# Kernel tuning notes

Measured on AMD Instinct MI355X. Metric: run time of the kernel, lower is better.

The kernel has to match this reference:

```python
import jax, jax.numpy as jnp
import numpy as np

N_NODES = 50000
N_EDGES = 800000
D_IN = 128
HIDDEN = [128, 128]
D_OUT = 64


def setup_inputs() -> dict:
    key = jax.random.key(0)
    ks = jax.random.split(key, 12)
    x = jax.random.normal(ks[0], (N_NODES, D_IN), dtype=jnp.float32)
    edge_index = jax.random.randint(ks[1], (2, N_EDGES), 0, N_NODES, dtype=jnp.int64)
    # SAGEConv params: lin_l acts on aggregated neighbors (has bias), lin_r on root
    def lin(k, fan_in, fan_out):
        s = 1.0 / np.sqrt(fan_in)
        return jax.random.uniform(k, (fan_in, fan_out), jnp.float32, -s, s)
    dims = [D_IN] + HIDDEN
    inp = {"x": x, "edge_index": edge_index}
    for i in range(len(HIDDEN)):
        inp[f"Wl{i}"] = lin(ks[2 + 3 * i], dims[i], dims[i + 1])
        inp[f"Wr{i}"] = lin(ks[3 + 3 * i], dims[i], dims[i + 1])
        inp[f"b{i}"] = jnp.zeros((dims[i + 1],), jnp.float32)
    inp["Wfc"] = lin(ks[10], HIDDEN[-1], D_OUT)
    inp["bfc"] = jnp.zeros((D_OUT,), jnp.float32)
    return inp


def _sage_conv(x, src, dst, n, Wl, Wr, b, deg_inv):
    # mean-aggregate source features into destination nodes
    agg = jax.ops.segment_sum(x[src], dst, num_segments=n) * deg_inv[:, None]
    return agg @ Wl + x @ Wr + b


def reference(x, edge_index, Wl0, Wr0, b0, Wl1, Wr1, b1, Wfc, bfc):
    src, dst = edge_index[0], edge_index[1]
    n = x.shape[0]
    deg = jax.ops.segment_sum(jnp.ones((src.shape[0],), x.dtype), dst, num_segments=n)
    deg_inv = 1.0 / jnp.maximum(deg, 1.0)
    h = jax.nn.relu(_sage_conv(x, src, dst, n, Wl0, Wr0, b0, deg_inv))
    # dropout p=0 / eval mode -> identity
    h = jax.nn.relu(_sage_conv(h, src, dst, n, Wl1, Wr1, b1, deg_inv))
    return h @ Wfc + bfc
```

## Files before the change

kernel.cpp:

```cpp
#include <hip/hip_runtime.h>
#include <hip/hip_bf16.h>

#define NN 50000
#define NE 800000
#define D 128
#define DOUT 64
#define PAD 64
#define BSH 8
#define NBUCK 196
#define CAP 4608
#define CHUNK 4096
#define N8 (NN * D / 8)

typedef __attribute__((ext_vector_type(8))) short short8;
typedef __attribute__((ext_vector_type(4))) float float4v;


__device__ inline unsigned short f2bf(float f) {
    union { float f; unsigned int i; } c; c.f = f;
    unsigned int u = c.i;
    return (unsigned short)((u + 0x7fffu + ((u >> 16) & 1u)) >> 16);
}
__device__ inline float bflo(unsigned int u) {
    union { unsigned int i; float f; } c; c.i = u << 16; return c.f;
}
__device__ inline float bfhi(unsigned int u) {
    union { unsigned int i; float f; } c; c.i = u & 0xffff0000u; return c.f;
}


struct PrepArgs {
    const float* W[5];
    unsigned short* P[5];
    int* gcur;
    const float* x;
    unsigned short* xb;
    unsigned short* zrow;
};

__global__ void prep(PrepArgs args) {
    int b = blockIdx.x;
    if (b < 36) {
        int idx = b * 256 + threadIdx.x;
        const float* W;
        unsigned short* P;
        int COLS, local;
        if (idx < 4 * 2048) {
            int wsel = idx >> 11;
            W = args.W[wsel]; P = args.P[wsel]; COLS = 128; local = idx & 2047;
        } else {
            W = args.W[4]; P = args.P[4]; COLS = 64; local = idx - 4 * 2048;
        }
        int CT = COLS >> 4;
        int lane = local & 63;
        int fi = local >> 6;
        int ct = fi % CT;
        int kstep = fi / CT;
        int krow = kstep * 32 + (lane >> 4) * 8;
        int col = ct * 16 + (lane & 15);
        unsigned short v[8];
#pragma unroll
        for (int j = 0; j < 8; ++j) v[j] = f2bf(W[(size_t)(krow + j) * COLS + col]);
        unsigned int w0 = v[0] | ((unsigned int)v[1] << 16);
        unsigned int w1 = v[2] | ((unsigned int)v[3] << 16);
        unsigned int w2 = v[4] | ((unsigned int)v[5] << 16);
        unsigned int w3 = v[6] | ((unsigned int)v[7] << 16);
        *(uint4*)(P + (size_t)local * 8) = make_uint4(w0, w1, w2, w3);
    } else if (b == 36) {
        if (threadIdx.x < NBUCK) args.gcur[threadIdx.x] = 0;
        if (threadIdx.x >= 224 && threadIdx.x < 240)
            *(uint4*)(args.zrow + (size_t)(threadIdx.x - 224) * 8) = make_uint4(0, 0, 0, 0);
    } else {
        int stride = (gridDim.x - 37) * 256;
        for (int i = (b - 37) * 256 + threadIdx.x; i < N8; i += stride) {
            const float4* p = (const float4*)args.x + (size_t)i * 2;
            float4 a = p[0], bb = p[1];
            unsigned int w0 = f2bf(a.x) | ((unsigned int)f2bf(a.y) << 16);
            unsigned int w1 = f2bf(a.z) | ((unsigned int)f2bf(a.w) << 16);
            unsigned int w2 = f2bf(bb.x) | ((unsigned int)f2bf(bb.y) << 16);
            unsigned int w3 = f2bf(bb.z) | ((unsigned int)f2bf(bb.w) << 16);
            *(uint4*)(args.xb + (size_t)i * 8) = make_uint4(w0, w1, w2, w3);
        }
    }
}


__global__ void bin_edges(const int* __restrict__ src, const int* __restrict__ dst,
                          int* __restrict__ gcur, unsigned int* __restrict__ binned, int e) {
    __shared__ int cnt[NBUCK];
    __shared__ int sh[256];
    __shared__ int baseg[NBUCK];
    __shared__ int lcur[NBUCK];
    __shared__ unsigned int buf[CHUNK];
    int tid = threadIdx.x;
    int base = blockIdx.x * CHUNK;
    for (int b = tid; b < NBUCK; b += 256) cnt[b] = 0;
    __syncthreads();
    unsigned int rec[16];
#pragma unroll
    for (int i = 0; i < 16; ++i) {
        int ei = base + i * 256 + tid;
        rec[i] = 0xffffffffu;
        if (ei < e) {
            unsigned int d = (unsigned int)dst[ei];
            unsigned int s = (unsigned int)src[ei];
            rec[i] = (d << 16) | s;
            atomicAdd(&cnt[d >> BSH], 1);
        }
    }
    __syncthreads();
    int v = (tid < NBUCK) ? cnt[tid] : 0;
    sh[tid] = v;
    __syncthreads();
    for (int off = 1; off < 256; off <<= 1) {
        int t = (tid >= off) ? sh[tid - off] : 0;
        __syncthreads();
        sh[tid] += t;
        __syncthreads();
    }
    if (tid < NBUCK) {
        baseg[tid] = atomicAdd(&gcur[tid], cnt[tid]);
        lcur[tid] = sh[tid] - cnt[tid];
    }
    __syncthreads();
    int total = sh[255];
#pragma unroll
    for (int i = 0; i < 16; ++i) {
        if (rec[i] != 0xffffffffu) {
            int b = rec[i] >> 24;
            int pos = atomicAdd(&lcur[b], 1);
            buf[pos] = rec[i];
        }
    }
    __syncthreads();
    for (int j = tid; j < total; j += 256) {
        unsigned int r = buf[j];
        int b = r >> 24;
        int gidx = baseg[b] + (j - (sh[b] - cnt[b]));
        if (gidx < CAP) binned[(size_t)b * CAP + gidx] = r;
    }
}


__global__ void scatter_bucket(const unsigned int* __restrict__ binned, const int* __restrict__ gcur,
                               unsigned short* __restrict__ eidx_pad, int* __restrict__ cursor) {
    __shared__ int cur[256];
    int b = blockIdx.x;
    int tid = threadIdx.x;
    if (tid < 256) cur[tid] = 0;
    __syncthreads();
    int count = gcur[b];
    if (count > CAP) count = CAP;
    const unsigned int* seg = binned + (size_t)b * CAP;
    for (int j = tid; j < count; j += 512) {
        unsigned int r = seg[j];
        int dl = (r >> 16) & 255;
        int slot = atomicAdd(&cur[dl], 1);
        if (slot < PAD)
            eidx_pad[((size_t)((b << BSH) + dl)) * PAD + slot] = (unsigned short)(r & 0xffffu);
    }
    __syncthreads();
    if (tid < 256) {
        int node = (b << BSH) + tid;
        if (node < NN) cursor[node] = (cur[tid] < PAD) ? cur[tid] : PAD;
    }
}


template <bool FUSEFC>
__global__ __launch_bounds__(256, 4)
void fused_layer(const unsigned short* __restrict__ feat,
                 const int* __restrict__ cursor, const unsigned short* __restrict__ eidx_pad,
                 const unsigned short* __restrict__ zrow,
                 const unsigned short* __restrict__ Pl, const unsigned short* __restrict__ Pr,
                 const float* __restrict__ bias,
                 const unsigned short* __restrict__ Pfc, const float* __restrict__ bfc,
                 unsigned short* __restrict__ outb, float* __restrict__ outf, int n) {
    __shared__ __align__(16) unsigned short As[64][136];

    int tid = threadIdx.x;
    int row0 = blockIdx.x * 64;

    {
        int g = tid >> 4;
        int l = tid & 15;
        int nbase = row0 + g * 4;
        int4 dv = *(const int4*)(cursor + nbase);
        const unsigned short* rbase = eidx_pad + (size_t)nbase * PAD;
        uint4 ia = *(const uint4*)(rbase);
        uint4 ib = *(const uint4*)(rbase + 8);
#pragma unroll
        for (int nn = 0; nn < 4; ++nn) {
            int r = g * 4 + nn;
            int node = nbase + nn;
            uint4 ca = ia, cb = ib;
            if (nn < 3) {
                ia = *(const uint4*)(rbase + (nn + 1) * PAD);
                ib = *(const uint4*)(rbase + (nn + 1) * PAD + 8);
            }
            int deg = 0;
            if (node < n) deg = ((const int*)&dv)[nn];
            float di = 1.0f / (float)(deg > 1 ? deg : 1);
            float acc[8] = {0.f, 0.f, 0.f, 0.f, 0.f, 0.f, 0.f, 0.f};
            {
                int id[16];
                id[0] = ca.x & 0xffff;  id[1] = ca.x >> 16;
                id[2] = ca.y & 0xffff;  id[3] = ca.y >> 16;
                id[4] = ca.z & 0xffff;  id[5] = ca.z >> 16;
                id[6] = ca.w & 0xffff;  id[7] = ca.w >> 16;
                id[8] = cb.x & 0xffff;  id[9] = cb.x >> 16;
                id[10] = cb.y & 0xffff; id[11] = cb.y >> 16;
                id[12] = cb.z & 0xffff; id[13] = cb.z >> 16;
                id[14] = cb.w & 0xffff; id[15] = cb.w >> 16;
                uint4 v[16];
#pragma unroll
                for (int k = 0; k < 16; ++k) {
                    const unsigned short* sp = (k < deg) ? (feat + (size_t)id[k] * D) : zrow;
                    v[k] = *(const uint4*)(sp + l * 8);
                }
#pragma unroll
                for (int k = 0; k < 16; ++k) {
                    acc[0] += bflo(v[k].x); acc[1] += bfhi(v[k].x);
                    acc[2] += bflo(v[k].y); acc[3] += bfhi(v[k].y);
                    acc[4] += bflo(v[k].z); acc[5] += bfhi(v[k].z);
                    acc[6] += bflo(v[k].w); acc[7] += bfhi(v[k].w);
                }
                const unsigned short* rowp = rbase + nn * PAD;
                int p = 16;
                while (p < deg) {
                    uint4 iv = *(const uint4*)(rowp + p);
                    int jd[8];
                    jd[0] = iv.x & 0xffff; jd[1] = iv.x >> 16;
                    jd[2] = iv.y & 0xffff; jd[3] = iv.y >> 16;
                    jd[4] = iv.z & 0xffff; jd[5] = iv.z >> 16;
                    jd[6] = iv.w & 0xffff; jd[7] = iv.w >> 16;
                    uint4 w[8];
#pragma unroll
                    for (int k = 0; k < 8; ++k) {
                        const unsigned short* sp = (p + k < deg) ? (feat + (size_t)jd[k] * D) : zrow;
                        w[k] = *(const uint4*)(sp + l * 8);
                    }
#pragma unroll
                    for (int k = 0; k < 8; ++k) {
                        acc[0] += bflo(w[k].x); acc[1] += bfhi(w[k].x);
                        acc[2] += bflo(w[k].y); acc[3] += bfhi(w[k].y);
                        acc[4] += bflo(w[k].z); acc[5] += bfhi(w[k].z);
                        acc[6] += bflo(w[k].w); acc[7] += bfhi(w[k].w);
                    }
                    p += 8;
                }
            }
            unsigned int w0 = f2bf(acc[0] * di) | ((unsigned int)f2bf(acc[1] * di) << 16);
            unsigned int w1 = f2bf(acc[2] * di) | ((unsigned int)f2bf(acc[3] * di) << 16);
            unsigned int w2 = f2bf(acc[4] * di) | ((unsigned int)f2bf(acc[5] * di) << 16);
            unsigned int w3 = f2bf(acc[6] * di) | ((unsigned int)f2bf(acc[7] * di) << 16);
            *(uint4*)&As[r][l * 8] = make_uint4(w0, w1, w2, w3);
        }
    }

    int wave = tid >> 6;
    int lane = tid & 63;
    int m16 = lane & 15;
    int quad = lane >> 4;
    int rt0 = (wave & 1) * 32;
    int ctb = (wave >> 1) * 4;

    float4v acc[2][4];
#pragma unroll
    for (int t = 0; t < 2; ++t)
#pragma unroll
        for (int c = 0; c < 4; ++c) acc[t][c] = (float4v){0.f, 0.f, 0.f, 0.f};

#pragma unroll
    for (int ks = 0; ks < 4; ++ks) {
        short8 xf[2];
#pragma unroll
        for (int t = 0; t < 2; ++t) {
            int row = row0 + rt0 + t * 16 + m16;
            short8 z = {0, 0, 0, 0, 0, 0, 0, 0};
            xf[t] = (row < n) ? *(const short8*)(feat + (size_t)row * D + ks * 32 + quad * 8) : z;
        }
#pragma unroll
        for (int c = 0; c < 4; ++c) {
            short8 bf = *(const short8*)(Pr + ((size_t)((ks * 8 + ctb + c) * 64 + lane)) * 8);
#pragma unroll
            for (int t = 0; t < 2; ++t)
                acc[t][c] = __builtin_amdgcn_mfma_f32_16x16x32_bf16(xf[t], bf, acc[t][c], 0, 0, 0);
        }
    }

    __syncthreads();

#pragma unroll
    for (int ks = 0; ks < 4; ++ks) {
        short8 af[2];
#pragma unroll
        for (int t = 0; t < 2; ++t)
            af[t] = *(const short8*)&As[rt0 + t * 16 + m16][ks * 32 + quad * 8];
#pragma unroll
        for (int c = 0; c < 4; ++c) {
            short8 bf = *(const short8*)(Pl + ((size_t)((ks * 8 + ctb + c) * 64 + lane)) * 8);
#pragma unroll
            for (int t = 0; t < 2; ++t)
                acc[t][c] = __builtin_amdgcn_mfma_f32_16x16x32_bf16(af[t], bf, acc[t][c], 0, 0, 0);
        }
    }

    if (!FUSEFC) {
#pragma unroll
        for (int t = 0; t < 2; ++t) {
#pragma unroll
            for (int c = 0; c < 4; ++c) {
                int col = (ctb + c) * 16 + m16;
                float bv = bias[col];
#pragma unroll
                for (int i = 0; i < 4; ++i) {
                    int row = row0 + rt0 + t * 16 + quad * 4 + i;
                    if (row < n)
                        outb[(size_t)row * D + col] = f2bf(fmaxf(acc[t][c][i] + bv, 0.f));
                }
            }
        }
    } else {
        __syncthreads();
#pragma unroll
        for (int t = 0; t < 2; ++t) {
#pragma unroll
            for (int c = 0; c < 4; ++c) {
                int col = (ctb + c) * 16 + m16;
                float bv = bias[col];
#pragma unroll
                for (int i = 0; i < 4; ++i) {
                    int row = rt0 + t * 16 + quad * 4 + i;
                    As[row][col] = f2bf(fmaxf(acc[t][c][i] + bv, 0.f));
                }
            }
        }
        __syncthreads();

        int ctbF = (wave >> 1) * 2;
        float4v acc2[2][2];
#pragma unroll
        for (int t = 0; t < 2; ++t)
#pragma unroll
            for (int c = 0; c < 2; ++c) acc2[t][c] = (float4v){0.f, 0.f, 0.f, 0.f};
#pragma unroll
        for (int ks = 0; ks < 4; ++ks) {
            short8 hf[2];
#pragma unroll
            for (int t = 0; t < 2; ++t)
                hf[t] = *(const short8*)&As[rt0 + t * 16 + m16][ks * 32 + quad * 8];
#pragma unroll
            for (int c = 0; c < 2; ++c) {
                short8 bf = *(const short8*)(Pfc + ((size_t)((ks * 4 + ctbF + c) * 64 + lane)) * 8);
#pragma unroll
                for (int t = 0; t < 2; ++t)
                    acc2[t][c] = __builtin_amdgcn_mfma_f32_16x16x32_bf16(hf[t], bf, acc2[t][c], 0, 0, 0);
            }
        }
#pragma unroll
        for (int t = 0; t < 2; ++t) {
#pragma unroll
            for (int c = 0; c < 2; ++c) {
                int col = (ctbF + c) * 16 + m16;
                float bv = bfc[col];
#pragma unroll
                for (int i = 0; i < 4; ++i) {
                    int row = row0 + rt0 + t * 16 + quad * 4 + i;
                    if (row < n)
                        outf[(size_t)row * DOUT + col] = acc2[t][c][i] + bv;
                }
            }
        }
    }
}


extern "C" void kernel_launch(void* const* d_in, const int* in_sizes, int n_in,
                              void* d_out, int out_size, void* d_ws, size_t ws_size,
                              hipStream_t stream) {
    const float* x   = (const float*)d_in[0];
    const int*   ei  = (const int*)d_in[1];
    const float* Wl0 = (const float*)d_in[2];
    const float* Wr0 = (const float*)d_in[3];
    const float* b0  = (const float*)d_in[4];
    const float* Wl1 = (const float*)d_in[5];
    const float* Wr1 = (const float*)d_in[6];
    const float* b1  = (const float*)d_in[7];
    const float* Wfc = (const float*)d_in[8];
    const float* bfc = (const float*)d_in[9];
    float* out = (float*)d_out;

    const int* src = ei;
    const int* dst = ei + NE;

    char* p = (char*)d_ws;
    auto carve = [&](size_t bytes) {
        char* q = p;
        p += (bytes + 255) & ~(size_t)255;
        return q;
    };
    int*            cursor   = (int*)carve(NN * sizeof(int));
    int*            gcur     = (int*)carve(NBUCK * sizeof(int));
    unsigned short* zrow     = (unsigned short*)carve(256);
    unsigned int*   binned   = (unsigned int*)carve((size_t)NBUCK * CAP * 4);
    unsigned short* eidx_pad = (unsigned short*)carve((size_t)NN * PAD * 2);
    unsigned short* xb   = (unsigned short*)carve((size_t)NN * D * 2);
    unsigned short* h0b  = (unsigned short*)carve((size_t)NN * D * 2);
    unsigned short* Wl0p = (unsigned short*)carve(D * D * 2);
    unsigned short* Wr0p = (unsigned short*)carve(D * D * 2);
    unsigned short* Wl1p = (unsigned short*)carve(D * D * 2);
    unsigned short* Wr1p = (unsigned short*)carve(D * D * 2);
    unsigned short* Wfcp = (unsigned short*)carve(D * DOUT * 2);

    PrepArgs pa;
    pa.W[0] = Wl0; pa.W[1] = Wr0; pa.W[2] = Wl1; pa.W[3] = Wr1; pa.W[4] = Wfc;
    pa.P[0] = Wl0p; pa.P[1] = Wr0p; pa.P[2] = Wl1p; pa.P[3] = Wr1p; pa.P[4] = Wfcp;
    pa.gcur = gcur;
    pa.x = x; pa.xb = xb;
    pa.zrow = zrow;
    prep<<<256, 256, 0, stream>>>(pa);

    const int BINB = (NE + CHUNK - 1) / CHUNK;
    bin_edges<<<BINB, 256, 0, stream>>>(src, dst, gcur, binned, NE);
    scatter_bucket<<<NBUCK, 512, 0, stream>>>(binned, gcur, eidx_pad, cursor);

    const int GB = (NN + 63) / 64;

    fused_layer<false><<<GB, 256, 0, stream>>>(xb, cursor, eidx_pad, zrow, Wl0p, Wr0p, b0,
                                               nullptr, nullptr, h0b, nullptr, NN);
    fused_layer<true><<<GB, 256, 0, stream>>>(h0b, cursor, eidx_pad, zrow, Wl1p, Wr1p, b1,
                                              Wfcp, bfc, nullptr, out, NN);
}
```

Baseline: 187.0 us.

## Merge prep and edge binning into one kernel using per-block bucket segments

Edge binning now writes each block's bucket records into a fixed-size private segment (SEGC slots per block per bucket) with per-block counts, instead of reserving space through global atomics on a gcur counter. That removes the need to zero gcur beforehand, so the binning blocks and the weight/x bf16 conversion blocks are folded into a single launch, dropping one kernel boundary. scatter_bucket then walks every block segment for its bucket, which adds some strided, partly empty reads. Edges beyond SEGC in any block/bucket pair are silently dropped, which is a correctness risk if a bucket gets skewed.

```diff
diff --git a/kernel.cpp b/kernel.cpp
--- a/kernel.cpp
+++ b/kernel.cpp
@@ -8,8 +8,9 @@
 #define PAD 64
 #define BSH 8
 #define NBUCK 196
-#define CAP 4608
 #define CHUNK 4096
+#define NBINB 196
+#define SEGC 56
 #define N8 (NN * D / 8)
 
 typedef __attribute__((ext_vector_type(8))) short short8;
@@ -29,139 +30,143 @@
 }
 
 
-struct PrepArgs {
+struct Stage1Args {
+    const int* src;
+    const int* dst;
+    unsigned int* binned;
+    int* cnts;
     const float* W[5];
     unsigned short* P[5];
-    int* gcur;
     const float* x;
     unsigned short* xb;
     unsigned short* zrow;
 };
 
-__global__ void prep(PrepArgs args) {
-    int b = blockIdx.x;
-    if (b < 36) {
-        int idx = b * 256 + threadIdx.x;
-        const float* W;
-        unsigned short* P;
-        int COLS, local;
-        if (idx < 4 * 2048) {
-            int wsel = idx >> 11;
-            W = args.W[wsel]; P = args.P[wsel]; COLS = 128; local = idx & 2047;
+__global__ void stage1(Stage1Args args) {
+    int blk = blockIdx.x;
+    int tid = threadIdx.x;
+    if (blk < NBINB) {
+        __shared__ int cnt[NBUCK];
+        __shared__ int sh[256];
+        __shared__ int lcur[NBUCK];
+        __shared__ unsigned int buf[CHUNK];
+        int base = blk * CHUNK;
+        for (int b = tid; b < NBUCK; b += 256) cnt[b] = 0;
+        __syncthreads();
+        unsigned int rec[16];
+#pragma unroll
+        for (int i = 0; i < 16; ++i) {
+            int ei = base + i * 256 + tid;
+            rec[i] = 0xffffffffu;
+            if (ei < NE) {
+                unsigned int d = (unsigned int)args.dst[ei];
+                unsigned int s = (unsigned int)args.src[ei];
+                rec[i] = (d << 16) | s;
+                atomicAdd(&cnt[d >> BSH], 1);
+            }
+        }
+        __syncthreads();
+        int v = (tid < NBUCK) ? cnt[tid] : 0;
+        sh[tid] = v;
+        __syncthreads();
+        for (int off = 1; off < 256; off <<= 1) {
+            int t = (tid >= off) ? sh[tid - off] : 0;
+            __syncthreads();
+            sh[tid] += t;
+            __syncthreads();
+        }
+        if (tid < NBUCK) {
+            lcur[tid] = sh[tid] - cnt[tid];
+            args.cnts[blk * NBUCK + tid] = (cnt[tid] < SEGC) ? cnt[tid] : SEGC;
+        }
+        __syncthreads();
+        int total = sh[255];
+#pragma unroll
+        for (int i = 0; i < 16; ++i) {
+            if (rec[i] != 0xffffffffu) {
+                int b = rec[i] >> 24;
+                int pos = atomicAdd(&lcur[b], 1);
+                buf[pos] = rec[i];
+            }
+        }
+        __syncthreads();
+        for (int j = tid; j < total; j += 256) {
+            unsigned int r = buf[j];
+            int q = r >> 24;
+            int k = j - (sh[q] - cnt[q]);
+            if (k < SEGC)
+                args.binned[((size_t)q * NBINB + blk) * SEGC + k] = r;
+        }
+    } else {
+        int b = blk - NBINB;
+        if (b < 36) {
+            int idx = b * 256 + tid;
+            const float* W;
+            unsigned short* P;
+            int COLS, local;
+            if (idx < 4 * 2048) {
+                int wsel = idx >> 11;
+                W = args.W[wsel]; P = args.P[wsel]; COLS = 128; local = idx & 2047;
+            } else {
+                W = args.W[4]; P = args.P[4]; COLS = 64; local = idx - 4 * 2048;
+            }
+            int CT = COLS >> 4;
+            int lane = local & 63;
+            int fi = local >> 6;
+            int ct = fi % CT;
+            int kstep = fi / CT;
+            int krow = kstep * 32 + (lane >> 4) * 8;
+            int col = ct * 16 + (lane & 15);
+            unsigned short v[8];
+#pragma unroll
+            for (int j = 0; j < 8; ++j) v[j] = f2bf(W[(size_t)(krow + j) * COLS + col]);
+            unsigned int w0 = v[0] | ((unsigned int)v[1] << 16);
+            unsigned int w1 = v[2] | ((unsigned int)v[3] << 16);
+            unsigned int w2 = v[4] | ((unsigned int)v[5] << 16);
+            unsigned int w3 = v[6] | ((unsigned int)v[7] << 16);
+            *(uint4*)(P + (size_t)local * 8) = make_uint4(w0, w1, w2, w3);
+            if (b == 0 && tid < 16)
+                *(uint4*)(args.zrow + (size_t)tid * 8) = make_uint4(0, 0, 0, 0);
         } else {
-            W = args.W[4]; P = args.P[4]; COLS = 64; local = idx - 4 * 2048;
-        }
-        int CT = COLS >> 4;
-        int lane = local & 63;
-        int fi = local >> 6;
-        int ct = fi % CT;
-        int kstep = fi / CT;
-        int krow = kstep * 32 + (lane >> 4) * 8;
-        int col = ct * 16 + (lane & 15);
-        unsigned short v[8];
-#pragma unroll
-        for (int j = 0; j < 8; ++j) v[j] = f2bf(W[(size_t)(krow + j) * COLS + col]);
-        unsigned int w0 = v[0] | ((unsigned int)v[1] << 16);
-        unsigned int w1 = v[2] | ((unsigned int)v[3] << 16);
-        unsigned int w2 = v[4] | ((unsigned int)v[5] << 16);
-        unsigned int w3 = v[6] | ((unsigned int)v[7] << 16);
-        *(uint4*)(P + (size_t)local * 8) = make_uint4(w0, w1, w2, w3);
-    } else if (b == 36) {
-        if (threadIdx.x < NBUCK) args.gcur[threadIdx.x] = 0;
-        if (threadIdx.x >= 224 && threadIdx.x < 240)
-            *(uint4*)(args.zrow + (size_t)(threadIdx.x - 224) * 8) = make_uint4(0, 0, 0, 0);
-    } else {
-        int stride = (gridDim.x - 37) * 256;
-        for (int i = (b - 37) * 256 + threadIdx.x; i < N8; i += stride) {
-            const float4* p = (const float4*)args.x + (size_t)i * 2;
-            float4 a = p[0], bb = p[1];
-            unsigned int w0 = f2bf(a.x) | ((unsigned int)f2bf(a.y) << 16);
-            unsigned int w1 = f2bf(a.z) | ((unsigned int)f2bf(a.w) << 16);
-            unsigned int w2 = f2bf(bb.x) | ((unsigned int)f2bf(bb.y) << 16);
-            unsigned int w3 = f2bf(bb.z) | ((unsigned int)f2bf(bb.w) << 16);
-            *(uint4*)(args.xb + (size_t)i * 8) = make_uint4(w0, w1, w2, w3);
-        }
-    }
-}
-
-
-__global__ void bin_edges(const int* __restrict__ src, const int* __restrict__ dst,
-                          int* __restrict__ gcur, unsigned int* __restrict__ binned, int e) {
-    __shared__ int cnt[NBUCK];
-    __shared__ int sh[256];
-    __shared__ int baseg[NBUCK];
-    __shared__ int lcur[NBUCK];
-    __shared__ unsigned int buf[CHUNK];
-    int tid = threadIdx.x;
-    int base = blockIdx.x * CHUNK;
-    for (int b = tid; b < NBUCK; b += 256) cnt[b] = 0;
-    __syncthreads();
-    unsigned int rec[16];
-#pragma unroll
-    for (int i = 0; i < 16; ++i) {
-        int ei = base + i * 256 + tid;
-        rec[i] = 0xffffffffu;
-        if (ei < e) {
-            unsigned int d = (unsigned int)dst[ei];
-            unsigned int s = (unsigned int)src[ei];
-            rec[i] = (d << 16) | s;
-            atomicAdd(&cnt[d >> BSH], 1);
-        }
-    }
-    __syncthreads();
-    int v = (tid < NBUCK) ? cnt[tid] : 0;
-    sh[tid] = v;
-    __syncthreads();
-    for (int off = 1; off < 256; off <<= 1) {
-        int t = (tid >= off) ? sh[tid - off] : 0;
-        __syncthreads();
-        sh[tid] += t;
-        __syncthreads();
-    }
-    if (tid < NBUCK) {
-        baseg[tid] = atomicAdd(&gcur[tid], cnt[tid]);
-        lcur[tid] = sh[tid] - cnt[tid];
-    }
-    __syncthreads();
-    int total = sh[255];
-#pragma unroll
-    for (int i = 0; i < 16; ++i) {
-        if (rec[i] != 0xffffffffu) {
-            int b = rec[i] >> 24;
-            int pos = atomicAdd(&lcur[b], 1);
-            buf[pos] = rec[i];
-        }
-    }
-    __syncthreads();
-    for (int j = tid; j < total; j += 256) {
-        unsigned int r = buf[j];
-        int b = r >> 24;
-        int gidx = baseg[b] + (j - (sh[b] - cnt[b]));
-        if (gidx < CAP) binned[(size_t)b * CAP + gidx] = r;
-    }
-}
-
-
-__global__ void scatter_bucket(const unsigned int* __restrict__ binned, const int* __restrict__ gcur,
+            int stride = (gridDim.x - NBINB - 36) * 256;
+            for (int i = (b - 36) * 256 + tid; i < N8; i += stride) {
+                const float4* p = (const float4*)args.x + (size_t)i * 2;
+                float4 a = p[0], bb = p[1];
+                unsigned int w0 = f2bf(a.x) | ((unsigned int)f2bf(a.y) << 16);
+                unsigned int w1 = f2bf(a.z) | ((unsigned int)f2bf(a.w) << 16);
+                unsigned int w2 = f2bf(bb.x) | ((unsigned int)f2bf(bb.y) << 16);
+                unsigned int w3 = f2bf(bb.z) | ((unsigned int)f2bf(bb.w) << 16);
+                *(uint4*)(args.xb + (size_t)i * 8) = make_uint4(w0, w1, w2, w3);
+            }
+        }
+    }
+}
+
+
+__global__ void scatter_bucket(const unsigned int* __restrict__ binned, const int* __restrict__ cnts,
                                unsigned short* __restrict__ eidx_pad, int* __restrict__ cursor) {
     __shared__ int cur[256];
-    int b = blockIdx.x;
+    __shared__ int segc[NBINB];
+    int q = blockIdx.x;
     int tid = threadIdx.x;
     if (tid < 256) cur[tid] = 0;
+    for (int s = tid; s < NBINB; s += 512) segc[s] = cnts[(size_t)s * NBUCK + q];
     __syncthreads();
-    int count = gcur[b];
-    if (count > CAP) count = CAP;
-    const unsigned int* seg = binned + (size_t)b * CAP;
-    for (int j = tid; j < count; j += 512) {
-        unsigned int r = seg[j];
-        int dl = (r >> 16) & 255;
-        int slot = atomicAdd(&cur[dl], 1);
-        if (slot < PAD)
-            eidx_pad[((size_t)((b << BSH) + dl)) * PAD + slot] = (unsigned short)(r & 0xffffu);
+    const unsigned int* bq = binned + (size_t)q * NBINB * SEGC;
+    for (int idx = tid; idx < NBINB * SEGC; idx += 512) {
+        int seg = idx / SEGC;
+        int k = idx - seg * SEGC;
+        if (k < segc[seg]) {
+            unsigned int r = bq[(size_t)seg * SEGC + k];
+            int dl = (r >> 16) & 255;
+            int slot = atomicAdd(&cur[dl], 1);
+            if (slot < PAD)
+                eidx_pad[((size_t)((q << BSH) + dl)) * PAD + slot] = (unsigned short)(r & 0xffffu);
+        }
     }
     __syncthreads();
     if (tid < 256) {
-        int node = (b << BSH) + tid;
+        int node = (q << BSH) + tid;
         if (node < NN) cursor[node] = (cur[tid] < PAD) ? cur[tid] : PAD;
     }
 }
@@ -401,9 +406,9 @@
         return q;
     };
     int*            cursor   = (int*)carve(NN * sizeof(int));
-    int*            gcur     = (int*)carve(NBUCK * sizeof(int));
+    int*            cnts     = (int*)carve((size_t)NBINB * NBUCK * sizeof(int));
     unsigned short* zrow     = (unsigned short*)carve(256);
-    unsigned int*   binned   = (unsigned int*)carve((size_t)NBUCK * CAP * 4);
+    unsigned int*   binned   = (unsigned int*)carve((size_t)NBUCK * NBINB * SEGC * 4);
     unsigned short* eidx_pad = (unsigned short*)carve((size_t)NN * PAD * 2);
     unsigned short* xb   = (unsigned short*)carve((size_t)NN * D * 2);
     unsigned short* h0b  = (unsigned short*)carve((size_t)NN * D * 2);
@@ -413,17 +418,15 @@
     unsigned short* Wr1p = (unsigned short*)carve(D * D * 2);
     unsigned short* Wfcp = (unsigned short*)carve(D * DOUT * 2);
 
-    PrepArgs pa;
-    pa.W[0] = Wl0; pa.W[1] = Wr0; pa.W[2] = Wl1; pa.W[3] = Wr1; pa.W[4] = Wfc;
-    pa.P[0] = Wl0p; pa.P[1] = Wr0p; pa.P[2] = Wl1p; pa.P[3] = Wr1p; pa.P[4] = Wfcp;
-    pa.gcur = gcur;
-    pa.x = x; pa.xb = xb;
-    pa.zrow = zrow;
-    prep<<<256, 256, 0, stream>>>(pa);
-
-    const int BINB = (NE + CHUNK - 1) / CHUNK;
-    bin_edges<<<BINB, 256, 0, stream>>>(src, dst, gcur, binned, NE);
-    scatter_bucket<<<NBUCK, 512, 0, stream>>>(binned, gcur, eidx_pad, cursor);
+    Stage1Args sa;
+    sa.src = src; sa.dst = dst;
+    sa.binned = binned; sa.cnts = cnts;
+    sa.W[0] = Wl0; sa.W[1] = Wr0; sa.W[2] = Wl1; sa.W[3] = Wr1; sa.W[4] = Wfc;
+    sa.P[0] = Wl0p; sa.P[1] = Wr0p; sa.P[2] = Wl1p; sa.P[3] = Wr1p; sa.P[4] = Wfcp;
+    sa.x = x; sa.xb = xb; sa.zrow = zrow;
+    stage1<<<NBINB + 256, 256, 0, stream>>>(sa);
+
+    scatter_bucket<<<NBUCK, 512, 0, stream>>>(binned, cnts, eidx_pad, cursor);
 
     const int GB = (NN + 63) / 64;
 
```

New measurement: 183.6 us. About the same (-1.8%).
